# Kernel optimization log

Hardware: AMD Instinct MI355X
Metric: run time of the kernel (lower is better)

Reference implementation:

```python
import jax, jax.numpy as jnp
import numpy as np

NEG_SLOPE = 0.2  # PyG GATConv default negative_slope


def gat_conv(x, src, dst, n_nodes, W, a_src, a_dst, b, concat):
    # x: [N, F_in], W: [F_in, H*C], a_src/a_dst: [H, C], b: [H*C] or [C]
    H, C = a_src.shape
    h = (x @ W).reshape(n_nodes, H, C)              # [N, H, C]
    e_s = jnp.sum(h * a_src, axis=-1)               # [N, H]
    e_d = jnp.sum(h * a_dst, axis=-1)               # [N, H]
    e = jax.nn.leaky_relu(e_s[src] + e_d[dst], NEG_SLOPE)  # [E, H]
    # segment softmax over incoming edges of each destination node
    m = jax.ops.segment_max(e, dst, num_segments=n_nodes)
    m = jnp.where(jnp.isfinite(m), m, 0.0)
    p = jnp.exp(e - m[dst])                         # [E, H]
    s = jax.ops.segment_sum(p, dst, num_segments=n_nodes)
    alpha = p / (s[dst] + 1e-16)                    # [E, H]
    out = jax.ops.segment_sum(h[src] * alpha[:, :, None], dst, num_segments=n_nodes)  # [N, H, C]
    out = out.reshape(n_nodes, H * C) if concat else out.mean(axis=1)
    return out + b


def setup_inputs() -> dict:
    key = jax.random.key(0)
    ks = jax.random.split(key, 20)
    N, E = 50000, 800000
    F_in, C, H = 128, 64, 4
    sc = 0.05
    inp = {
        "x": jax.random.normal(ks[0], (N, F_in), dtype=jnp.float32),
        "edge_index": jax.random.randint(ks[1], (2, E), 0, N, dtype=jnp.int64),
        # conv1: F_in -> C x H heads, concat
        "W1": jax.random.normal(ks[2], (F_in, H * C), dtype=jnp.float32) * sc,
        "a1_src": jax.random.normal(ks[3], (H, C), dtype=jnp.float32) * sc,
        "a1_dst": jax.random.normal(ks[4], (H, C), dtype=jnp.float32) * sc,
        "b1": jnp.zeros((H * C,), dtype=jnp.float32),
        # conv2: H*C -> C x H heads, concat
        "W2": jax.random.normal(ks[5], (H * C, H * C), dtype=jnp.float32) * sc,
        "a2_src": jax.random.normal(ks[6], (H, C), dtype=jnp.float32) * sc,
        "a2_dst": jax.random.normal(ks[7], (H, C), dtype=jnp.float32) * sc,
        "b2": jnp.zeros((H * C,), dtype=jnp.float32),
        # conv3: H*C -> C, 1 head, concat=False (mean)
        "W3": jax.random.normal(ks[8], (H * C, C), dtype=jnp.float32) * sc,
        "a3_src": jax.random.normal(ks[9], (1, C), dtype=jnp.float32) * sc,
        "a3_dst": jax.random.normal(ks[10], (1, C), dtype=jnp.float32) * sc,
        "b3": jnp.zeros((C,), dtype=jnp.float32),
        # node classification head: C -> 2
        "cls_W": jax.random.normal(ks[11], (C, 2), dtype=jnp.float32) * sc,
        "cls_b": jnp.zeros((2,), dtype=jnp.float32),
    }
    return inp


def reference(x, edge_index, W1, a1_src, a1_dst, b1, W2, a2_src, a2_dst, b2,
              W3, a3_src, a3_dst, b3, cls_W, cls_b):
    N = x.shape[0]
    # PyG GATConv default: add self loops
    loop = jnp.arange(N, dtype=edge_index.dtype)
    ei = jnp.concatenate([edge_index, jnp.stack([loop, loop])], axis=1)
    src, dst = ei[0], ei[1]

    h = jax.nn.elu(gat_conv(x, src, dst, N, W1, a1_src, a1_dst, b1, concat=True))
    h = jax.nn.elu(gat_conv(h, src, dst, N, W2, a2_src, a2_dst, b2, concat=True))
    h = gat_conv(h, src, dst, N, W3, a3_src, a3_dst, b3, concat=False)  # [N, C]

    node_output = h @ cls_W + cls_b  # [N, 2]
    link_embedding = h               # [N, C]
    return node_output, link_embedding
```

## Files before the change

### kernel.cpp

```cpp
#include <hip/hip_runtime.h>
#include <math.h>


typedef unsigned short ushort;
typedef __attribute__((ext_vector_type(8))) short bf16x8;
typedef __attribute__((ext_vector_type(4))) float f32x4;

#define LOG2E 1.4426950408889634f

static __device__ __forceinline__ ushort f2bf(float f) {
    unsigned x = __float_as_uint(f);
    unsigned r = (x + 0x7FFF + ((x >> 16) & 1)) >> 16;
    return (ushort)r;
}
static __device__ __forceinline__ float bf2f(ushort u) {
    return __uint_as_float(((unsigned)u) << 16);
}


__global__ void count_deg(const int* __restrict__ ei, int E, int* __restrict__ deg) {
    int i = blockIdx.x * blockDim.x + threadIdx.x;
    int stride = gridDim.x * blockDim.x;
    for (int e = i; e < E; e += stride) {
        int d = ei[E + e];
        atomicAdd(&deg[d], 1);
    }
}

__global__ void scan_local(const int* __restrict__ deg, int* __restrict__ offsets,
                           int* __restrict__ blockSums, int N) {
    int tid = threadIdx.x;
    int lane = tid & 63;
    int wv = tid >> 6;
    int base = blockIdx.x * 1024 + tid * 4;
    int v[4];
#pragma unroll
    for (int j = 0; j < 4; ++j) {
        int idx = base + j;
        v[j] = (idx < N) ? ((deg[idx] + 1 + 7) & ~7) : 0;
    }
    int tsum = v[0] + v[1] + v[2] + v[3];
    int inc = tsum;
#pragma unroll
    for (int off = 1; off < 64; off <<= 1) {
        int u = __shfl_up(inc, off);
        if (lane >= off) inc += u;
    }
    __shared__ int wtot[4];
    if (lane == 63) wtot[wv] = inc;
    __syncthreads();
    int wbase = 0;
#pragma unroll
    for (int w = 0; w < 4; ++w)
        if (w < wv) wbase += wtot[w];
    int run = wbase + inc - tsum;
#pragma unroll
    for (int j = 0; j < 4; ++j) {
        int idx = base + j;
        if (idx < N) offsets[idx] = run;
        run += v[j];
    }
    if (tid == 255) blockSums[blockIdx.x] = wbase + inc;
}

__global__ void scan_blocks(const int* __restrict__ blockSums, int* __restrict__ blockBase,
                            int* __restrict__ offsets, int N, int nblk) {
    int lane = threadIdx.x & 63;
    int v = (lane < nblk) ? blockSums[lane] : 0;
    int inc = v;
#pragma unroll
    for (int off = 1; off < 64; off <<= 1) {
        int u = __shfl_up(inc, off);
        if (lane >= off) inc += u;
    }
    if (lane < nblk) blockBase[lane] = inc - v;
    if (lane == 63) offsets[N] = inc;
}

__global__ void scan_add(int* __restrict__ offsets, const int* __restrict__ blockBase, int N) {
    int i = blockIdx.x * blockDim.x + threadIdx.x;
    if (i < N) offsets[i] += blockBase[i >> 10];
}

__global__ void fill_sent(int* __restrict__ csr_src, int cap, int N) {
    int i = blockIdx.x * blockDim.x + threadIdx.x;
    if (i < cap) csr_src[i] = N;
}

__global__ void fill_self(const int* __restrict__ offsets, int* __restrict__ counter,
                          int* __restrict__ csr_src, int N) {
    int i = blockIdx.x * blockDim.x + threadIdx.x;
    if (i < N) {
        csr_src[offsets[i]] = i;
        counter[i] = 1;
    }
}

__global__ void fill_edges(const int* __restrict__ ei, int E,
                           const int* __restrict__ offsets, int* __restrict__ counter,
                           int* __restrict__ csr_src) {
    int i = blockIdx.x * blockDim.x + threadIdx.x;
    int stride = gridDim.x * blockDim.x;
    for (int e = i; e < E; e += stride) {
        int s = ei[e];
        int d = ei[E + e];
        int pos = offsets[d] + atomicAdd(&counter[d], 1);
        csr_src[pos] = s;
    }
}


__global__ void xsplit(const float* __restrict__ X, ushort* __restrict__ Xh,
                       ushort* __restrict__ Xl, int total4) {
    int i = blockIdx.x * blockDim.x + threadIdx.x;
    if (i >= total4) return;
    float4 v = *(const float4*)(X + (size_t)i * 4);
    ushort4 h, l;
    h.x = f2bf(v.x); l.x = f2bf(v.x - bf2f(h.x));
    h.y = f2bf(v.y); l.y = f2bf(v.y - bf2f(h.y));
    h.z = f2bf(v.z); l.z = f2bf(v.z - bf2f(h.z));
    h.w = f2bf(v.w); l.w = f2bf(v.w - bf2f(h.w));
    *(ushort4*)(Xh + (size_t)i * 4) = h;
    *(ushort4*)(Xl + (size_t)i * 4) = l;
}

__global__ void wtrans_bf(const float* __restrict__ W, ushort* __restrict__ Wt,
                          int K, int N) {
    int id = blockIdx.x * blockDim.x + threadIdx.x;
    if (id >= K * N) return;
    int k = id % K, n = id / K;
    Wt[id] = f2bf(W[(size_t)k * N + n]);
}

__global__ void init_sent(ushort* __restrict__ hb, float* __restrict__ e_s4,
                          float* __restrict__ e_s3, int N) {
    int t = threadIdx.x;
    if (t < 64) {
        ushort4 z = {0, 0, 0, 0};
        *(ushort4*)(hb + (size_t)N * 256 + t * 4) = z;
    } else if (t < 68) {
        e_s4[(size_t)N * 4 + (t - 64)] = -1e30f;
    } else if (t == 68) {
        e_s3[N] = -1e30f;
    }
}


template<int BM, int BN, int WM, int WN, int THREADS, int H>
__global__ __launch_bounds__(THREADS) void gemm_mfma(const ushort* __restrict__ Ah,
                                                     const ushort* __restrict__ Al,
                                                     const ushort* __restrict__ Bh,
                                                     ushort* __restrict__ Cb,
                                                     float* __restrict__ e_s,
                                                     float* __restrict__ e_d,
                                                     const float* __restrict__ a_src,
                                                     const float* __restrict__ a_dst,
                                                     int M, int N, int K) {
    constexpr int BK = 32, PAD = 8;
    constexpr int MI = BM / WM / 16;
    constexpr int NI = BN / WN / 16;
    static_assert(WM * WN * 64 == THREADS, "wave grid mismatch");
    __shared__ ushort As[2][BM][BK + PAD];
    __shared__ ushort Bs[BN][BK + PAD];

    int tid = threadIdx.x;
    int lane = tid & 63;
    int wid = tid >> 6;
    int fr = lane & 15;
    int fg = lane >> 4;
    int wm0 = (wid / WN) * (BM / WM);
    int wn0 = (wid % WN) * (BN / WN);
    int mBase = blockIdx.x * BM;
    int nBase = blockIdx.y * BN;

    f32x4 acc[MI][NI];
#pragma unroll
    for (int mi = 0; mi < MI; ++mi)
#pragma unroll
        for (int ni = 0; ni < NI; ++ni) acc[mi][ni] = (f32x4)0.0f;

    constexpr int ACH = BM * BK / 8;
    constexpr int BCH = BN * BK / 8;

    const int KI = K / BK;
    for (int t = 0; t < KI; ++t) {
        int k0 = t * BK;
        for (int q = tid; q < ACH; q += THREADS) {
            int row = q >> 2;
            int sl = (q & 3) * 8;
            int gm = mBase + row;
            if (gm >= M) gm = M - 1;
            size_t off = (size_t)gm * K + k0 + sl;
            *(bf16x8*)&As[0][row][sl] = *(const bf16x8*)(Ah + off);
            *(bf16x8*)&As[1][row][sl] = *(const bf16x8*)(Al + off);
        }
        for (int q = tid; q < BCH; q += THREADS) {
            int row = q >> 2;
            int sl = (q & 3) * 8;
            size_t off = (size_t)(nBase + row) * K + k0 + sl;
            *(bf16x8*)&Bs[row][sl] = *(const bf16x8*)(Bh + off);
        }
        __syncthreads();

        bf16x8 afh[MI], afl[MI], bfh[NI];
#pragma unroll
        for (int mi = 0; mi < MI; ++mi) {
            afh[mi] = *(const bf16x8*)&As[0][wm0 + mi * 16 + fr][fg * 8];
            afl[mi] = *(const bf16x8*)&As[1][wm0 + mi * 16 + fr][fg * 8];
        }
#pragma unroll
        for (int ni = 0; ni < NI; ++ni)
            bfh[ni] = *(const bf16x8*)&Bs[wn0 + ni * 16 + fr][fg * 8];
#pragma unroll
        for (int mi = 0; mi < MI; ++mi)
#pragma unroll
            for (int ni = 0; ni < NI; ++ni) {
                acc[mi][ni] = __builtin_amdgcn_mfma_f32_16x16x32_bf16(
                    afh[mi], bfh[ni], acc[mi][ni], 0, 0, 0);
                acc[mi][ni] = __builtin_amdgcn_mfma_f32_16x16x32_bf16(
                    afl[mi], bfh[ni], acc[mi][ni], 0, 0, 0);
            }
        __syncthreads();
    }

#pragma unroll
    for (int mi = 0; mi < MI; ++mi) {
#pragma unroll
        for (int j = 0; j < 4; ++j) {
            int gm = mBase + wm0 + mi * 16 + fg * 4 + j;
            if (gm >= M) continue;
#pragma unroll
            for (int ni = 0; ni < NI; ++ni) {
                int gn = nBase + wn0 + ni * 16 + fr;
                Cb[(size_t)gm * N + gn] = f2bf(acc[mi][ni][j]);
            }
        }
    }

    float asv[NI], adv[NI];
#pragma unroll
    for (int ni = 0; ni < NI; ++ni) {
        int col = wn0 + ni * 16 + fr;
        asv[ni] = a_src[col];
        adv[ni] = a_dst[col];
    }
    if constexpr (WN == H) {
        const int head = wn0 / (BN / H);
#pragma unroll
        for (int mi = 0; mi < MI; ++mi) {
#pragma unroll
            for (int j = 0; j < 4; ++j) {
                float ps = 0.0f, pd = 0.0f;
#pragma unroll
                for (int ni = 0; ni < NI; ++ni) {
                    ps += acc[mi][ni][j] * asv[ni];
                    pd += acc[mi][ni][j] * adv[ni];
                }
#pragma unroll
                for (int off = 1; off <= 8; off <<= 1) {
                    ps += __shfl_xor(ps, off);
                    pd += __shfl_xor(pd, off);
                }
                int gm = mBase + wm0 + mi * 16 + fg * 4 + j;
                if (fr == 0 && gm < M) {
                    e_s[(size_t)gm * H + head] = ps * LOG2E;
                    e_d[(size_t)gm * H + head] = pd * LOG2E;
                }
            }
        }
    } else {
        __shared__ float esb[WN][BM];
        __shared__ float edb[WN][BM];
        int wc = wid % WN;
#pragma unroll
        for (int mi = 0; mi < MI; ++mi) {
#pragma unroll
            for (int j = 0; j < 4; ++j) {
                float ps = 0.0f, pd = 0.0f;
#pragma unroll
                for (int ni = 0; ni < NI; ++ni) {
                    ps += acc[mi][ni][j] * asv[ni];
                    pd += acc[mi][ni][j] * adv[ni];
                }
#pragma unroll
                for (int off = 1; off <= 8; off <<= 1) {
                    ps += __shfl_xor(ps, off);
                    pd += __shfl_xor(pd, off);
                }
                if (fr == 0) {
                    int lr = wm0 + mi * 16 + fg * 4 + j;
                    esb[wc][lr] = ps;
                    edb[wc][lr] = pd;
                }
            }
        }
        __syncthreads();
        if (tid < BM) {
            int gm = mBase + tid;
            if (gm < M) {
                float ps = 0.0f, pd = 0.0f;
#pragma unroll
                for (int wcc = 0; wcc < WN; ++wcc) {
                    ps += esb[wcc][tid];
                    pd += edb[wcc][tid];
                }
                e_s[gm] = ps * LOG2E;
                e_d[gm] = pd * LOG2E;
            }
        }
        if (blockIdx.x == 0 && tid < 16) {
            ushort4 z = {0, 0, 0, 0};
            *(ushort4*)(Cb + (size_t)M * N + tid * 4) = z;
        }
    }
}


template<int HC, int H, bool ELU, bool SPLIT, bool CLS>
__global__ void aggregate(const ushort* __restrict__ hb,
                          const float* __restrict__ e_s, const float* __restrict__ e_d,
                          const int* __restrict__ offsets, const int* __restrict__ csr_src,
                          const float* __restrict__ bias,
                          float* __restrict__ out,
                          ushort* __restrict__ oh, ushort* __restrict__ ol,
                          const float* __restrict__ clsW, const float* __restrict__ clsB,
                          float* __restrict__ outN, int N) {
    int wid = (int)((blockIdx.x * (size_t)blockDim.x + threadIdx.x) >> 6);
    int lane = threadIdx.x & 63;
    if (wid >= N) return;
    constexpr int VEC = HC / 64;
    constexpr int C = HC / H;
    constexpr int ROWSH = (HC == 256) ? 9 : 7;
    int hd = (lane * VEC) / C;
    float ed = e_d[(size_t)wid * H + hd];
    int beg = offsets[wid], end = offsets[wid + 1];
    const char* hbB = (const char*)hb;
    const char* esB = (const char*)e_s;
    unsigned laneOff = (unsigned)lane * (VEC * 2);

    float s = 0.0f;
    float acc[VEC];
#pragma unroll
    for (int j = 0; j < VEC; ++j) acc[j] = 0.0f;

    for (int k = beg; k < end; k += 8) {
        int4 c0 = *(const int4*)(csr_src + k);
        int4 c1 = *(const int4*)(csr_src + k + 4);
        int sidx[8] = {c0.x, c0.y, c0.z, c0.w, c1.x, c1.y, c1.z, c1.w};
        float e[8];
#pragma unroll
        for (int u = 0; u < 8; ++u)
            e[u] = *(const float*)(esB + (((unsigned)(sidx[u] * H + hd)) << 2));
        ushort4 hv4[8];
        ushort  hv1[8];
        if constexpr (VEC == 4) {
#pragma unroll
            for (int u = 0; u < 8; ++u)
                hv4[u] = *(const ushort4*)(hbB + (((unsigned)sidx[u]) << ROWSH) + laneOff);
        } else {
#pragma unroll
            for (int u = 0; u < 8; ++u)
                hv1[u] = *(const ushort*)(hbB + (((unsigned)sidx[u]) << ROWSH) + laneOff);
        }
        float p[8];
        float psum = 0.0f;
#pragma unroll
        for (int u = 0; u < 8; ++u) {
            float t = e[u] + ed;
            t = (t >= 0.0f) ? t : 0.2f * t;
            p[u] = __builtin_amdgcn_exp2f(t);
            psum += p[u];
        }
        s += psum;
        if constexpr (VEC == 4) {
#pragma unroll
            for (int u = 0; u < 8; ++u) {
                acc[0] += p[u] * bf2f(hv4[u].x);
                acc[1] += p[u] * bf2f(hv4[u].y);
                acc[2] += p[u] * bf2f(hv4[u].z);
                acc[3] += p[u] * bf2f(hv4[u].w);
            }
        } else {
#pragma unroll
            for (int u = 0; u < 8; ++u) acc[0] += p[u] * bf2f(hv1[u]);
        }
    }
    float inv = 1.0f / (s + 1e-16f);
    float o[VEC];
#pragma unroll
    for (int j = 0; j < VEC; ++j) {
        int f = lane * VEC + j;
        o[j] = acc[j] * inv + bias[f];
        if constexpr (ELU) o[j] = (o[j] > 0.0f) ? o[j] : expm1f(o[j]);
    }
    if constexpr (SPLIT) {
        if constexpr (VEC == 4) {
            ushort4 h4, l4;
            h4.x = f2bf(o[0]); l4.x = f2bf(o[0] - bf2f(h4.x));
            h4.y = f2bf(o[1]); l4.y = f2bf(o[1] - bf2f(h4.y));
            h4.z = f2bf(o[2]); l4.z = f2bf(o[2] - bf2f(h4.z));
            h4.w = f2bf(o[3]); l4.w = f2bf(o[3] - bf2f(h4.w));
            *(ushort4*)(oh + (size_t)wid * HC + lane * 4) = h4;
            *(ushort4*)(ol + (size_t)wid * HC + lane * 4) = l4;
        } else {
            ushort h1 = f2bf(o[0]);
            oh[(size_t)wid * HC + lane] = h1;
            ol[(size_t)wid * HC + lane] = f2bf(o[0] - bf2f(h1));
        }
    } else {
#pragma unroll
        for (int j = 0; j < VEC; ++j)
            out[(size_t)wid * HC + lane * VEC + j] = o[j];
    }
    if constexpr (CLS) {
        float p0 = o[0] * clsW[lane * 2 + 0];
        float p1 = o[0] * clsW[lane * 2 + 1];
#pragma unroll
        for (int off = 1; off <= 32; off <<= 1) {
            p0 += __shfl_xor(p0, off);
            p1 += __shfl_xor(p1, off);
        }
        if (lane == 0) {
            outN[(size_t)wid * 2 + 0] = p0 + clsB[0];
            outN[(size_t)wid * 2 + 1] = p1 + clsB[1];
        }
    }
}


extern "C" void kernel_launch(void* const* d_in, const int* in_sizes, int n_in,
                              void* d_out, int out_size, void* d_ws, size_t ws_size,
                              hipStream_t stream) {
    const float* x      = (const float*)d_in[0];
    const int*   ei     = (const int*)d_in[1];
    const float* W1     = (const float*)d_in[2];
    const float* a1_src = (const float*)d_in[3];
    const float* a1_dst = (const float*)d_in[4];
    const float* b1     = (const float*)d_in[5];
    const float* W2     = (const float*)d_in[6];
    const float* a2_src = (const float*)d_in[7];
    const float* a2_dst = (const float*)d_in[8];
    const float* b2     = (const float*)d_in[9];
    const float* W3     = (const float*)d_in[10];
    const float* a3_src = (const float*)d_in[11];
    const float* a3_dst = (const float*)d_in[12];
    const float* b3     = (const float*)d_in[13];
    const float* cls_W  = (const float*)d_in[14];
    const float* cls_b  = (const float*)d_in[15];

    const int N = in_sizes[0] / 128;
    const int E = in_sizes[1] / 2;
    const int ETcap = E + 8 * N + 64;
    const int HC = 256;
    const int nScanBlk = (N + 1023) / 1024;

    char* w = (char*)d_ws;
    auto carve = [&](size_t bytes) {
        char* p = w;
        w += (bytes + 255) & ~(size_t)255;
        return p;
    };
    int*    deg     = (int*)   carve((size_t)N * 4);
    int*    counter = (int*)   carve((size_t)N * 4);
    int*    offsets = (int*)   carve((size_t)(N + 1) * 4);
    int*    csr_src = (int*)   carve((size_t)ETcap * 4);
    int*    blkSums = (int*)   carve((size_t)64 * 4);
    int*    blkBase = (int*)   carve((size_t)64 * 4);
    float*  e_s     = (float*) carve((size_t)(N + 1) * 4 * 4);
    float*  e_d     = (float*) carve((size_t)N * 4 * 4);
    float*  e_s3    = (float*) carve((size_t)(N + 1) * 4);
    float*  e_d3    = (float*) carve((size_t)N * 4);
    ushort* hb      = (ushort*)carve((size_t)(N + 1) * HC * 2);
    ushort* Ahi     = (ushort*)carve((size_t)N * HC * 2);
    ushort* Alo     = (ushort*)carve((size_t)N * HC * 2);
    ushort* W1t     = (ushort*)carve((size_t)128 * 256 * 2);
    ushort* W2t     = (ushort*)carve((size_t)256 * 256 * 2);
    ushort* W3t     = (ushort*)carve((size_t)256 * 64 * 2);
    (void)ws_size;

    float* out_node = (float*)d_out;
    float* out_link = (float*)d_out + 2 * (size_t)N;

    hipMemsetAsync(deg, 0, (size_t)N * 4, stream);
    int eblocks = (E + 255) / 256;
    if (eblocks > 2048) eblocks = 2048;
    count_deg<<<eblocks, 256, 0, stream>>>(ei, E, deg);
    scan_local<<<nScanBlk, 256, 0, stream>>>(deg, offsets, blkSums, N);
    scan_blocks<<<1, 64, 0, stream>>>(blkSums, blkBase, offsets, N, nScanBlk);
    scan_add<<<(N + 255) / 256, 256, 0, stream>>>(offsets, blkBase, N);
    fill_sent<<<(ETcap + 255) / 256, 256, 0, stream>>>(csr_src, ETcap, N);
    fill_self<<<(N + 255) / 256, 256, 0, stream>>>(offsets, counter, csr_src, N);
    fill_edges<<<eblocks, 256, 0, stream>>>(ei, E, offsets, counter, csr_src);

    xsplit<<<(N * 128 / 4 + 255) / 256, 256, 0, stream>>>(x, Ahi, Alo, N * 128 / 4);
    wtrans_bf<<<(128 * 256 + 255) / 256, 256, 0, stream>>>(W1, W1t, 128, 256);
    wtrans_bf<<<(256 * 256 + 255) / 256, 256, 0, stream>>>(W2, W2t, 256, 256);
    wtrans_bf<<<(256 * 64 + 255) / 256, 256, 0, stream>>>(W3, W3t, 256, 64);
    init_sent<<<1, 256, 0, stream>>>(hb, e_s, e_s3, N);

    dim3 g12((N + 63) / 64, 1);
    dim3 g3((N + 63) / 64, 1);
    int nodeBlocks = (N + 3) / 4;

    gemm_mfma<64, 256, 2, 4, 512, 4><<<g12, 512, 0, stream>>>(
        Ahi, Alo, W1t, hb, e_s, e_d, a1_src, a1_dst, N, 256, 128);
    aggregate<256, 4, true, true, false><<<nodeBlocks, 256, 0, stream>>>(
        hb, e_s, e_d, offsets, csr_src, b1, nullptr, Ahi, Alo,
        nullptr, nullptr, nullptr, N);
    gemm_mfma<64, 256, 2, 4, 512, 4><<<g12, 512, 0, stream>>>(
        Ahi, Alo, W2t, hb, e_s, e_d, a2_src, a2_dst, N, 256, 256);
    aggregate<256, 4, true, true, false><<<nodeBlocks, 256, 0, stream>>>(
        hb, e_s, e_d, offsets, csr_src, b2, nullptr, Ahi, Alo,
        nullptr, nullptr, nullptr, N);
    gemm_mfma<64, 64, 4, 2, 512, 1><<<g3, 512, 0, stream>>>(
        Ahi, Alo, W3t, hb, e_s3, e_d3, a3_src, a3_dst, N, 64, 256);
    aggregate<64, 1, false, false, true><<<nodeBlocks, 256, 0, stream>>>(
        hb, e_s3, e_d3, offsets, csr_src, b3, out_link, nullptr, nullptr,
        cls_W, cls_b, out_node, N);
}
```

Measured before the change: 356.1 us.

## Double-buffer aggregate gathers and merge small setup kernels

The aggregate loop is rewritten as a two-stage software pipeline: the next batch of 8 neighbour indices, scores and bf16 feature rows is loaded while the current batch is computed. Accumulation uses packed float2 vectors so the hardware can issue packed FMAs, and leaky-relu becomes a fmax. Separately, scan_add is folded into fill_self, and the three weight transposes plus sentinel init become one launch. This cuts launch count and hides gather latency, at the cost of higher register pressure from holding two buffers per wave.

```diff
diff --git a/kernel.cpp b/kernel.cpp
--- a/kernel.cpp
+++ b/kernel.cpp
@@ -5,6 +5,7 @@
 typedef unsigned short ushort;
 typedef __attribute__((ext_vector_type(8))) short bf16x8;
 typedef __attribute__((ext_vector_type(4))) float f32x4;
+typedef __attribute__((ext_vector_type(2))) float f32x2;
 
 #define LOG2E 1.4426950408889634f
 
@@ -77,21 +78,18 @@
     if (lane == 63) offsets[N] = inc;
 }
 
-__global__ void scan_add(int* __restrict__ offsets, const int* __restrict__ blockBase, int N) {
-    int i = blockIdx.x * blockDim.x + threadIdx.x;
-    if (i < N) offsets[i] += blockBase[i >> 10];
-}
-
 __global__ void fill_sent(int* __restrict__ csr_src, int cap, int N) {
     int i = blockIdx.x * blockDim.x + threadIdx.x;
     if (i < cap) csr_src[i] = N;
 }
 
-__global__ void fill_self(const int* __restrict__ offsets, int* __restrict__ counter,
-                          int* __restrict__ csr_src, int N) {
+__global__ void scan_add_fill(int* __restrict__ offsets, const int* __restrict__ blockBase,
+                              int* __restrict__ counter, int* __restrict__ csr_src, int N) {
     int i = blockIdx.x * blockDim.x + threadIdx.x;
     if (i < N) {
-        csr_src[offsets[i]] = i;
+        int o = offsets[i] + blockBase[i >> 10];
+        offsets[i] = o;
+        csr_src[o] = i;
         counter[i] = 1;
     }
 }
@@ -124,25 +122,40 @@
     *(ushort4*)(Xl + (size_t)i * 4) = l;
 }
 
-__global__ void wtrans_bf(const float* __restrict__ W, ushort* __restrict__ Wt,
-                          int K, int N) {
+__global__ void prep_misc(const float* __restrict__ W1, const float* __restrict__ W2,
+                          const float* __restrict__ W3,
+                          ushort* __restrict__ W1t, ushort* __restrict__ W2t,
+                          ushort* __restrict__ W3t,
+                          ushort* __restrict__ hb, float* __restrict__ e_s4,
+                          float* __restrict__ e_s3, int N) {
     int id = blockIdx.x * blockDim.x + threadIdx.x;
-    if (id >= K * N) return;
-    int k = id % K, n = id / K;
-    Wt[id] = f2bf(W[(size_t)k * N + n]);
-}
-
-__global__ void init_sent(ushort* __restrict__ hb, float* __restrict__ e_s4,
-                          float* __restrict__ e_s3, int N) {
-    int t = threadIdx.x;
-    if (t < 64) {
+    if (id < 32768) {
+        int k = id % 128, n = id / 128;
+        W1t[id] = f2bf(W1[(size_t)k * 256 + n]);
+        return;
+    }
+    id -= 32768;
+    if (id < 65536) {
+        int k = id % 256, n = id / 256;
+        W2t[id] = f2bf(W2[(size_t)k * 256 + n]);
+        return;
+    }
+    id -= 65536;
+    if (id < 16384) {
+        int k = id % 256, n = id / 256;
+        W3t[id] = f2bf(W3[(size_t)k * 64 + n]);
+        return;
+    }
+    id -= 16384;
+    if (id < 64) {
         ushort4 z = {0, 0, 0, 0};
-        *(ushort4*)(hb + (size_t)N * 256 + t * 4) = z;
-    } else if (t < 68) {
-        e_s4[(size_t)N * 4 + (t - 64)] = -1e30f;
-    } else if (t == 68) {
-        e_s3[N] = -1e30f;
-    }
+        *(ushort4*)(hb + (size_t)N * 256 + id * 4) = z;
+        return;
+    }
+    id -= 64;
+    if (id < 4) { e_s4[(size_t)N * 4 + id] = -1e30f; return; }
+    id -= 4;
+    if (id == 0) e_s3[N] = -1e30f;
 }
 
 
@@ -315,6 +328,56 @@
     }
 }
 
+
+#define AGG_LOAD(S, kk)                                                        \
+    do {                                                                       \
+        int4 q0 = *(const int4*)(csr_src + (kk));                              \
+        int4 q1 = *(const int4*)(csr_src + (kk) + 4);                          \
+        int sx[8] = {q0.x, q0.y, q0.z, q0.w, q1.x, q1.y, q1.z, q1.w};          \
+        _Pragma("unroll")                                                      \
+        for (int u = 0; u < 8; ++u)                                            \
+            eb##S[u] = *(const float*)(esB + (((unsigned)(sx[u] * H + hd)) << 2)); \
+        if constexpr (VEC == 4) {                                              \
+            _Pragma("unroll")                                                  \
+            for (int u = 0; u < 8; ++u)                                        \
+                hv##S[u] = *(const uint2*)(hbB + (((unsigned)sx[u]) << ROWSH) + laneOff); \
+        } else {                                                               \
+            _Pragma("unroll")                                                  \
+            for (int u = 0; u < 8; ++u)                                        \
+                hs##S[u] = *(const ushort*)(hbB + (((unsigned)sx[u]) << ROWSH) + laneOff); \
+        }                                                                      \
+    } while (0)
+
+#define AGG_COMPUTE(S)                                                         \
+    do {                                                                       \
+        float p[8];                                                            \
+        float ps = 0.0f;                                                       \
+        _Pragma("unroll")                                                      \
+        for (int u = 0; u < 8; ++u) {                                          \
+            float t = eb##S[u] + ed;                                           \
+            t = fmaxf(t, 0.2f * t);                                            \
+            p[u] = __builtin_amdgcn_exp2f(t);                                  \
+            ps += p[u];                                                        \
+        }                                                                      \
+        s += ps;                                                               \
+        if constexpr (VEC == 4) {                                              \
+            _Pragma("unroll")                                                  \
+            for (int u = 0; u < 8; ++u) {                                      \
+                uint2 wv_ = hv##S[u];                                          \
+                f32x2 a_, b_;                                                  \
+                a_[0] = __uint_as_float(wv_.x << 16);                          \
+                a_[1] = __uint_as_float(wv_.x & 0xffff0000u);                  \
+                b_[0] = __uint_as_float(wv_.y << 16);                          \
+                b_[1] = __uint_as_float(wv_.y & 0xffff0000u);                  \
+                acc01 += p[u] * a_;                                            \
+                acc23 += p[u] * b_;                                            \
+            }                                                                  \
+        } else {                                                               \
+            _Pragma("unroll")                                                  \
+            for (int u = 0; u < 8; ++u)                                        \
+                acc0 += p[u] * bf2f(hs##S[u]);                                 \
+        }                                                                      \
+    } while (0)
 
 template<int HC, int H, bool ELU, bool SPLIT, bool CLS>
 __global__ void aggregate(const ushort* __restrict__ hb,
@@ -339,58 +402,47 @@
     unsigned laneOff = (unsigned)lane * (VEC * 2);
 
     float s = 0.0f;
-    float acc[VEC];
-#pragma unroll
-    for (int j = 0; j < VEC; ++j) acc[j] = 0.0f;
-
-    for (int k = beg; k < end; k += 8) {
-        int4 c0 = *(const int4*)(csr_src + k);
-        int4 c1 = *(const int4*)(csr_src + k + 4);
-        int sidx[8] = {c0.x, c0.y, c0.z, c0.w, c1.x, c1.y, c1.z, c1.w};
-        float e[8];
-#pragma unroll
-        for (int u = 0; u < 8; ++u)
-            e[u] = *(const float*)(esB + (((unsigned)(sidx[u] * H + hd)) << 2));
-        ushort4 hv4[8];
-        ushort  hv1[8];
-        if constexpr (VEC == 4) {
-#pragma unroll
-            for (int u = 0; u < 8; ++u)
-                hv4[u] = *(const ushort4*)(hbB + (((unsigned)sidx[u]) << ROWSH) + laneOff);
-        } else {
-#pragma unroll
-            for (int u = 0; u < 8; ++u)
-                hv1[u] = *(const ushort*)(hbB + (((unsigned)sidx[u]) << ROWSH) + laneOff);
-        }
-        float p[8];
-        float psum = 0.0f;
-#pragma unroll
-        for (int u = 0; u < 8; ++u) {
-            float t = e[u] + ed;
-            t = (t >= 0.0f) ? t : 0.2f * t;
-            p[u] = __builtin_amdgcn_exp2f(t);
-            psum += p[u];
-        }
-        s += psum;
-        if constexpr (VEC == 4) {
-#pragma unroll
-            for (int u = 0; u < 8; ++u) {
-                acc[0] += p[u] * bf2f(hv4[u].x);
-                acc[1] += p[u] * bf2f(hv4[u].y);
-                acc[2] += p[u] * bf2f(hv4[u].z);
-                acc[3] += p[u] * bf2f(hv4[u].w);
+    f32x2 acc01 = {0.0f, 0.0f}, acc23 = {0.0f, 0.0f};
+    float acc0 = 0.0f;
+
+    float eb0[8], eb1[8];
+    uint2 hv0[8], hv1[8];
+    ushort hs0[8], hs1[8];
+
+    AGG_LOAD(0, beg);
+    int k = beg;
+    while (true) {
+        int kn = k + 8;
+        if (kn < end) {
+            AGG_LOAD(1, kn);
+            AGG_COMPUTE(0);
+            k = kn;
+            kn += 8;
+            if (kn < end) {
+                AGG_LOAD(0, kn);
+                AGG_COMPUTE(1);
+                k = kn;
+            } else {
+                AGG_COMPUTE(1);
+                break;
             }
         } else {
-#pragma unroll
-            for (int u = 0; u < 8; ++u) acc[0] += p[u] * bf2f(hv1[u]);
-        }
-    }
+            AGG_COMPUTE(0);
+            break;
+        }
+    }
+
     float inv = 1.0f / (s + 1e-16f);
     float o[VEC];
+    if constexpr (VEC == 4) {
+        o[0] = acc01[0]; o[1] = acc01[1]; o[2] = acc23[0]; o[3] = acc23[1];
+    } else {
+        o[0] = acc0;
+    }
 #pragma unroll
     for (int j = 0; j < VEC; ++j) {
         int f = lane * VEC + j;
-        o[j] = acc[j] * inv + bias[f];
+        o[j] = o[j] * inv + bias[f];
         if constexpr (ELU) o[j] = (o[j] > 0.0f) ? o[j] : expm1f(o[j]);
     }
     if constexpr (SPLIT) {
@@ -487,16 +539,13 @@
     count_deg<<<eblocks, 256, 0, stream>>>(ei, E, deg);
     scan_local<<<nScanBlk, 256, 0, stream>>>(deg, offsets, blkSums, N);
     scan_blocks<<<1, 64, 0, stream>>>(blkSums, blkBase, offsets, N, nScanBlk);
-    scan_add<<<(N + 255) / 256, 256, 0, stream>>>(offsets, blkBase, N);
     fill_sent<<<(ETcap + 255) / 256, 256, 0, stream>>>(csr_src, ETcap, N);
-    fill_self<<<(N + 255) / 256, 256, 0, stream>>>(offsets, counter, csr_src, N);
+    scan_add_fill<<<(N + 255) / 256, 256, 0, stream>>>(offsets, blkBase, counter, csr_src, N);
     fill_edges<<<eblocks, 256, 0, stream>>>(ei, E, offsets, counter, csr_src);
 
     xsplit<<<(N * 128 / 4 + 255) / 256, 256, 0, stream>>>(x, Ahi, Alo, N * 128 / 4);
-    wtrans_bf<<<(128 * 256 + 255) / 256, 256, 0, stream>>>(W1, W1t, 128, 256);
-    wtrans_bf<<<(256 * 256 + 255) / 256, 256, 0, stream>>>(W2, W2t, 256, 256);
-    wtrans_bf<<<(256 * 64 + 255) / 256, 256, 0, stream>>>(W3, W3t, 256, 64);
-    init_sent<<<1, 256, 0, stream>>>(hb, e_s, e_s3, N);
+    prep_misc<<<(32768 + 65536 + 16384 + 69 + 255) / 256, 256, 0, stream>>>(
+        W1, W2, W3, W1t, W2t, W3t, hb, e_s, e_s3, N);
 
     dim3 g12((N + 63) / 64, 1);
     dim3 g3((N + 63) / 64, 1);
```

Measured after the change: 377.2 us. 1.06x slower.
